# Optimization experiments

Measured on AMD Instinct MI355X. Metric: run time of the kernel, lower is better.

## Reference

```python
import jax, jax.numpy as jnp
import numpy as np

N_HEADS = 16

def setup_inputs() -> dict:
    key = jax.random.key(0)
    k1, k2, k3 = jax.random.split(key, 3)
    d = 1024
    x = jax.random.normal(k1, (2, 2048, d), dtype=jnp.float32)
    W_in = jax.random.normal(k2, (d, 3 * d), dtype=jnp.float32) * (d ** -0.5)
    W_out = jax.random.normal(k3, (d, d), dtype=jnp.float32) * (d ** -0.5)
    return {"x": x, "W_in": W_in, "W_out": W_out}

def reference(x, W_in, W_out):
    B, S, D = x.shape
    H = N_HEADS
    Dh = D // H
    qkv = x @ W_in                                  # [B,S,3D]
    q, k, v = jnp.split(qkv, 3, axis=-1)
    # [B,S,D] -> [B,H,S,Dh]
    q = q.reshape(B, S, H, Dh).transpose(0, 2, 1, 3)
    k = k.reshape(B, S, H, Dh).transpose(0, 2, 1, 3)
    v = v.reshape(B, S, H, Dh).transpose(0, 2, 1, 3)
    scores = jnp.einsum('bhqd,bhkd->bhqk', q, k)    # [B,H,S,S]
    causal = jnp.triu(jnp.ones((S, S), dtype=bool), k=1)
    scores = jnp.where(causal, -jnp.inf, scores)
    scores = scores / jnp.sqrt(jnp.asarray(Dh, scores.dtype))
    attn = jax.nn.softmax(scores, axis=-1)
    out = jnp.einsum('bhqk,bhkd->bhqd', attn, v)    # [B,H,S,Dh]
    out = out.transpose(0, 2, 1, 3).reshape(B, S, D)
    return out @ W_out
```

## Files before the change

### kernel.cpp

```cpp
#include <hip/hip_runtime.h>
#include <cstdint>
#include <cstddef>

typedef __bf16 bf16;
typedef bf16  bf16x4  __attribute__((ext_vector_type(4)));
typedef bf16  bf16x8  __attribute__((ext_vector_type(8)));
typedef float floatx4 __attribute__((ext_vector_type(4)));

#define BATCH 2
#define SEQ   2048
#define DIM   1024
#define NH    16
#define DH    64
#define D3    3072
#define MROWS 4096

__device__ __forceinline__ void gld16(void* lds, const void* gptr) {
  __builtin_amdgcn_global_load_lds(
      (const __attribute__((address_space(1))) unsigned int*)gptr,
      (__attribute__((address_space(3))) unsigned int*)lds, 16, 0, 0);
}

__global__ __launch_bounds__(256) void k_prep(const float4* __restrict__ x,
                                              bf16* __restrict__ xb,
                                              const float* __restrict__ Wi,
                                              bf16* __restrict__ wti,
                                              const float* __restrict__ Wo,
                                              bf16* __restrict__ wto) {
  __shared__ float tile[32][33];
  const int bid = blockIdx.x;
  if (bid < 4096) {
    int i = bid * 256 + threadIdx.x;
    float4 v = x[i];
    bf16x4 o;
    o.x = (bf16)v.x; o.y = (bf16)v.y; o.z = (bf16)v.z; o.w = (bf16)v.w;
    *(bf16x4*)(xb + (size_t)i * 4) = o;
    return;
  }
  const float* W; bf16* Wt; int N, id;
  if (bid < 7168) { W = Wi; Wt = wti; N = 3072; id = bid - 4096; }
  else            { W = Wo; Wt = wto; N = 1024; id = bid - 7168; }
  const int nb = N / 32;
  int n0 = (id % nb) * 32, k0 = (id / nb) * 32;
  int tx = threadIdx.x & 31, ty = threadIdx.x >> 5;
#pragma unroll
  for (int i = 0; i < 4; i++)
    tile[ty + i * 8][tx] = W[(size_t)(k0 + ty + i * 8) * N + n0 + tx];
  __syncthreads();
#pragma unroll
  for (int i = 0; i < 4; i++)
    Wt[(size_t)(n0 + ty + i * 8) * 1024 + k0 + tx] = (bf16)tile[tx][ty + i * 8];
}

__global__ __launch_bounds__(256, 2) void k_gemm1(const bf16* __restrict__ A,
                                                  const bf16* __restrict__ Bt,
                                                  bf16* __restrict__ qk,
                                                  bf16* __restrict__ vt) {
  constexpr int K = DIM;
  constexpr int nk = K / 64;
  __shared__ __align__(16) bf16 As[2][128 * 64];
  __shared__ __align__(16) bf16 Bs[2][192 * 64];

  const int t = threadIdx.x, l = t & 63, w = t >> 6;
  const int q = l >> 4, mm = l & 15;
  const int wm = w >> 1, wn = w & 1;

  const int xcd = blockIdx.x & 7, j = blockIdx.x >> 3;
  const int by = ((xcd >> 1) << 3) + (j >> 3);
  const int bx = ((xcd & 1) << 3) + (j & 7);
  const int m0 = by * 128, n0 = bx * 192;

  auto stA = [&](int T, int up) {
    const int bp = T & 1;
#pragma unroll
    for (int i = 0; i < 2; i++) {
      int c = t + i * 256;
      int rl = c >> 3, pos = c & 7;
      int row = ((rl >> 5) << 6) + (up << 5) + (rl & 31);
      int gs = pos ^ (row & 7);
      gld16((char*)(As[bp] + row * 64 + pos * 8),
            A + (size_t)(m0 + row) * K + T * 64 + gs * 8);
    }
  };
  auto stB = [&](int T, int up) {
    const int bp = T & 1;
#pragma unroll
    for (int i = 0; i < 3; i++) {
      int c = t + i * 256;
      int rl = c >> 3, pos = c & 7;
      int row = up * 96 + rl;
      int gs = pos ^ (row & 7);
      gld16((char*)(Bs[bp] + row * 64 + pos * 8),
            Bt + (size_t)(n0 + row) * K + T * 64 + gs * 8);
    }
  };

  floatx4 acc[4][6] = {};

  stA(0, 0); stB(0, 0); stA(0, 1); stB(0, 1);
  stA(1, 0); stB(1, 0);

  for (int T = 0; T < nk; T++) {
    const int bp = T & 1;
    if (T + 1 < nk)
      asm volatile("s_waitcnt vmcnt(5)\n\ts_barrier" ::: "memory");
    else
      asm volatile("s_waitcnt vmcnt(0)\n\ts_barrier" ::: "memory");

    const bf16* Ab = As[bp] + wm * 64 * 64;
    const bf16* Bb = Bs[bp] + wn * 96 * 64;
    bf16x8 a0[2][2], a1[2][2], b0[3][2], b1[3][2];

#pragma unroll
    for (int mt = 0; mt < 2; mt++)
#pragma unroll
      for (int kk = 0; kk < 2; kk++)
        a0[mt][kk] = *(const bf16x8*)(Ab + (size_t)(mt * 16 + mm) * 64 +
                                      ((kk * 4 + q) ^ (mm & 7)) * 8);
#pragma unroll
    for (int nt = 0; nt < 3; nt++)
#pragma unroll
      for (int kk = 0; kk < 2; kk++)
        b0[nt][kk] = *(const bf16x8*)(Bb + (size_t)(nt * 16 + mm) * 64 +
                                      ((kk * 4 + q) ^ (mm & 7)) * 8);
    if (T + 1 < nk) stA(T + 1, 1);
    asm volatile("s_barrier" ::: "memory");
    __builtin_amdgcn_s_setprio(1);
#pragma unroll
    for (int mt = 0; mt < 2; mt++)
#pragma unroll
      for (int nt = 0; nt < 3; nt++)
#pragma unroll
        for (int kk = 0; kk < 2; kk++)
          acc[mt][nt] = __builtin_amdgcn_mfma_f32_16x16x32_bf16(
              a0[mt][kk], b0[nt][kk], acc[mt][nt], 0, 0, 0);
    __builtin_amdgcn_s_setprio(0);
    asm volatile("s_barrier" ::: "memory");

#pragma unroll
    for (int nt = 0; nt < 3; nt++)
#pragma unroll
      for (int kk = 0; kk < 2; kk++)
        b1[nt][kk] = *(const bf16x8*)(Bb + (size_t)((3 + nt) * 16 + mm) * 64 +
                                      ((kk * 4 + q) ^ (mm & 7)) * 8);
    if (T + 1 < nk) stB(T + 1, 1);
    asm volatile("s_barrier" ::: "memory");
    __builtin_amdgcn_s_setprio(1);
#pragma unroll
    for (int mt = 0; mt < 2; mt++)
#pragma unroll
      for (int nt = 0; nt < 3; nt++)
#pragma unroll
        for (int kk = 0; kk < 2; kk++)
          acc[mt][3 + nt] = __builtin_amdgcn_mfma_f32_16x16x32_bf16(
              a0[mt][kk], b1[nt][kk], acc[mt][3 + nt], 0, 0, 0);
    __builtin_amdgcn_s_setprio(0);
    asm volatile("s_barrier" ::: "memory");

#pragma unroll
    for (int mt = 0; mt < 2; mt++)
#pragma unroll
      for (int kk = 0; kk < 2; kk++)
        a1[mt][kk] = *(const bf16x8*)(Ab + (size_t)(32 + mt * 16 + mm) * 64 +
                                      ((kk * 4 + q) ^ (mm & 7)) * 8);
    if (T + 2 < nk) stA(T + 2, 0);
    asm volatile("s_barrier" ::: "memory");
    __builtin_amdgcn_s_setprio(1);
#pragma unroll
    for (int mt = 0; mt < 2; mt++)
#pragma unroll
      for (int nt = 0; nt < 3; nt++)
#pragma unroll
        for (int kk = 0; kk < 2; kk++)
          acc[2 + mt][nt] = __builtin_amdgcn_mfma_f32_16x16x32_bf16(
              a1[mt][kk], b0[nt][kk], acc[2 + mt][nt], 0, 0, 0);
    __builtin_amdgcn_s_setprio(0);
    asm volatile("s_barrier" ::: "memory");

    if (T + 2 < nk) stB(T + 2, 0);
    asm volatile("s_barrier" ::: "memory");
    __builtin_amdgcn_s_setprio(1);
#pragma unroll
    for (int mt = 0; mt < 2; mt++)
#pragma unroll
      for (int nt = 0; nt < 3; nt++)
#pragma unroll
        for (int kk = 0; kk < 2; kk++)
          acc[2 + mt][3 + nt] = __builtin_amdgcn_mfma_f32_16x16x32_bf16(
              a1[mt][kk], b1[nt][kk], acc[2 + mt][3 + nt], 0, 0, 0);
    __builtin_amdgcn_s_setprio(0);
  }

#pragma unroll
  for (int mt = 0; mt < 4; mt++)
#pragma unroll
    for (int nt = 0; nt < 6; nt++) {
      int row = m0 + wm * 64 + mt * 16 + q * 4;
      int col = n0 + wn * 96 + nt * 16 + mm;
      if (col < 2048) {
#pragma unroll
        for (int r = 0; r < 4; r++)
          qk[(size_t)(row + r) * 2048 + col] = (bf16)acc[mt][nt][r];
      } else {
        int d = col - 2048;
        int hh = d >> 6, dh = d & 63;
#pragma unroll
        for (int r = 0; r < 4; r++) {
          int rr = row + r;
          int bb = rr >> 11, s = rr & 2047;
          vt[((size_t)(bb * 16 + hh) * 64 + dh) * SEQ + s] = (bf16)acc[mt][nt][r];
        }
      }
    }
}

__global__ __launch_bounds__(256, 2) void k_gemm2(const bf16* __restrict__ A,
                                                  const bf16* __restrict__ Bt,
                                                  float* __restrict__ C) {
  constexpr int K = DIM;
  constexpr int nk = K / 64;
  constexpr int N = DIM;
  __shared__ __align__(16) bf16 As[3][128 * 64];
  __shared__ __align__(16) bf16 Bs[3][64 * 64];

  const int t = threadIdx.x, l = t & 63, w = t >> 6;
  const int q = l >> 4, mm = l & 15;
  const int wm = w >> 1, wn = w & 1;

  const int xcd = blockIdx.x & 7, j = blockIdx.x >> 3;
  const int by = ((xcd >> 1) << 3) + (j >> 3);
  const int bx = ((xcd & 1) << 3) + (j & 7);
  const int m0 = by * 128, n0 = bx * 64;

  auto stA2 = [&](int T) {
    const int bp = T % 3;
#pragma unroll
    for (int i = 0; i < 4; i++) {
      int c = t + i * 256;
      int row = c >> 3, pos = c & 7;
      int gs = pos ^ (row & 7);
      gld16((char*)(As[bp] + row * 64 + pos * 8),
            A + (size_t)(m0 + row) * K + T * 64 + gs * 8);
    }
  };
  auto stB2 = [&](int T) {
    const int bp = T % 3;
#pragma unroll
    for (int i = 0; i < 2; i++) {
      int c = t + i * 256;
      int row = c >> 3, pos = c & 7;
      int gs = pos ^ (row & 7);
      gld16((char*)(Bs[bp] + row * 64 + pos * 8),
            Bt + (size_t)(n0 + row) * K + T * 64 + gs * 8);
    }
  };

  floatx4 acc[4][2] = {};

  stA2(0); stB2(0);
  stA2(1); stB2(1);

  for (int T = 0; T < nk; T++) {
    const int bp = T % 3;
    if (T + 1 < nk)
      asm volatile("s_waitcnt vmcnt(6)\n\ts_barrier" ::: "memory");
    else
      asm volatile("s_waitcnt vmcnt(0)\n\ts_barrier" ::: "memory");

    const bf16* Ab = As[bp] + wm * 64 * 64;
    const bf16* Bb = Bs[bp] + wn * 32 * 64;
    bf16x8 af[4][2], bf[2][2];

#pragma unroll
    for (int mt = 0; mt < 2; mt++)
#pragma unroll
      for (int kk = 0; kk < 2; kk++)
        af[mt][kk] = *(const bf16x8*)(Ab + (size_t)(mt * 16 + mm) * 64 +
                                      ((kk * 4 + q) ^ (mm & 7)) * 8);
#pragma unroll
    for (int nt = 0; nt < 2; nt++)
#pragma unroll
      for (int kk = 0; kk < 2; kk++)
        bf[nt][kk] = *(const bf16x8*)(Bb + (size_t)(nt * 16 + mm) * 64 +
                                      ((kk * 4 + q) ^ (mm & 7)) * 8);
    if (T + 2 < nk) stA2(T + 2);
    asm volatile("s_barrier" ::: "memory");
    __builtin_amdgcn_s_setprio(1);
#pragma unroll
    for (int mt = 0; mt < 2; mt++)
#pragma unroll
      for (int nt = 0; nt < 2; nt++)
#pragma unroll
        for (int kk = 0; kk < 2; kk++)
          acc[mt][nt] = __builtin_amdgcn_mfma_f32_16x16x32_bf16(
              af[mt][kk], bf[nt][kk], acc[mt][nt], 0, 0, 0);
    __builtin_amdgcn_s_setprio(0);
    asm volatile("s_barrier" ::: "memory");

#pragma unroll
    for (int mt = 0; mt < 2; mt++)
#pragma unroll
      for (int kk = 0; kk < 2; kk++)
        af[2 + mt][kk] = *(const bf16x8*)(Ab + (size_t)(32 + mt * 16 + mm) * 64 +
                                          ((kk * 4 + q) ^ (mm & 7)) * 8);
    if (T + 2 < nk) stB2(T + 2);
    asm volatile("s_barrier" ::: "memory");
    __builtin_amdgcn_s_setprio(1);
#pragma unroll
    for (int mt = 0; mt < 2; mt++)
#pragma unroll
      for (int nt = 0; nt < 2; nt++)
#pragma unroll
        for (int kk = 0; kk < 2; kk++)
          acc[2 + mt][nt] = __builtin_amdgcn_mfma_f32_16x16x32_bf16(
              af[2 + mt][kk], bf[nt][kk], acc[2 + mt][nt], 0, 0, 0);
    __builtin_amdgcn_s_setprio(0);
  }

#pragma unroll
  for (int mt = 0; mt < 4; mt++)
#pragma unroll
    for (int nt = 0; nt < 2; nt++) {
      int row = m0 + wm * 64 + mt * 16 + q * 4;
      int col = n0 + wn * 32 + nt * 16 + mm;
#pragma unroll
      for (int r = 0; r < 4; r++)
        C[(size_t)(row + r) * N + col] = acc[mt][nt][r];
    }
}

__global__ __launch_bounds__(256, 4) void k_attn(const bf16* __restrict__ qk,
                                                 const bf16* __restrict__ vt,
                                                 bf16* __restrict__ out) {
  const int bx = blockIdx.x;
  const int qt = 31 - (bx >> 5);
  const int bh = bx & 31;
  const int b = bh >> 4, h = bh & 15;
  const int t = threadIdx.x, l = t & 63, w = t >> 6;
  const int q4 = l >> 4, mm = l & 15;
  const int sw = (mm >> 1) & 3;

  __shared__ __align__(16) char lds[8192 + 16384 + 16384];
  bf16* Qs = (bf16*)lds;
  bf16* Ps = (bf16*)lds;
  bf16* Ks = (bf16*)(lds + 8192);
  bf16* Vs = (bf16*)(lds + 8192 + 16384);

  const size_t qkbase = (size_t)b * SEQ * 2048;
  const size_t vtbase = (size_t)bh * 64 * SEQ;

  auto stage = [&](int kt) {
    const int bp = kt & 1;
#pragma unroll
    for (int i = 0; i < 2; i++) {
      int row = t >> 2, pos = t & 3;
      int g = pos ^ ((row >> 1) & 3);
      gld16((char*)(Ks + bp * 4096) + ((size_t)t + i * 256) * 16,
            qk + qkbase + (size_t)(kt * 64 + row) * 2048 + 1024 + h * 64 + i * 32 + g * 8);
    }
#pragma unroll
    for (int i = 0; i < 2; i++) {
      int c = t + i * 256;
      int vr = c >> 3, vc = c & 7;
      int src = vc ^ (vr & 7);
      gld16((char*)(Vs + bp * 4096) + (size_t)c * 16,
            vt + vtbase + (size_t)vr * SEQ + kt * 64 + src * 8);
    }
  };

  {
    int row = t >> 2, col = (t & 3) * 8;
#pragma unroll
    for (int i = 0; i < 2; i++)
      gld16((char*)Qs + ((size_t)t + i * 256) * 16,
            qk + qkbase + (size_t)(qt * 64 + row) * 2048 + h * 64 + i * 32 + col);
  }
  stage(0);
  __syncthreads();
  bf16x8 qf[2];
#pragma unroll
  for (int ks = 0; ks < 2; ks++) {
    qf[ks] = *(const bf16x8*)(Qs + (size_t)(ks * 64 + w * 16 + mm) * 32 + q4 * 8);
#pragma unroll
    for (int j = 0; j < 8; j++)
      qf[ks][j] = (bf16)((float)qf[ks][j] * 0.18033688f);
  }
  __syncthreads();

  float l_i = 0.f;
  floatx4 oaccT[4] = {};
  const int qloc = w * 16 + mm;
  const float FM = 24.0f;

  bf16* Pw = Ps + (size_t)w * 640;

  for (int kt = 0; kt <= qt; kt++) {
    if (kt < qt) stage(kt + 1);
    const bf16* Kb = Ks + (kt & 1) * 4096;
    const bf16* Vb = Vs + (kt & 1) * 4096;

    floatx4 sacc[4] = {};
#pragma unroll
    for (int ks = 0; ks < 2; ks++)
#pragma unroll
      for (int ct = 0; ct < 4; ct++) {
        bf16x8 kf = *(const bf16x8*)(Kb + (size_t)(ks * 64 + ct * 16 + mm) * 32 + (q4 ^ sw) * 8);
        sacc[ct] = __builtin_amdgcn_mfma_f32_16x16x32_bf16(kf, qf[ks], sacc[ct], 0, 0, 0);
      }

    bf16x4 pk[4];
    float rsum = 0.f;
    if (kt == qt) {
#pragma unroll
      for (int ct = 0; ct < 4; ct++)
#pragma unroll
        for (int r = 0; r < 4; r++) {
          float e = (ct * 16 + q4 * 4 + r > qloc)
                        ? 0.f : __builtin_amdgcn_exp2f(sacc[ct][r] - FM);
          pk[ct][r] = (bf16)e;
          rsum += e;
        }
    } else {
#pragma unroll
      for (int ct = 0; ct < 4; ct++)
#pragma unroll
        for (int r = 0; r < 4; r++) {
          float e = __builtin_amdgcn_exp2f(sacc[ct][r] - FM);
          pk[ct][r] = (bf16)e;
          rsum += e;
        }
    }
    rsum += __shfl_xor(rsum, 16, 64);
    rsum += __shfl_xor(rsum, 32, 64);
    l_i += rsum;

#pragma unroll
    for (int ks = 0; ks < 2; ks++) {
      *(bf16x4*)(Pw + (size_t)mm * 40 + q4 * 4)      = pk[ks * 2 + 0];
      *(bf16x4*)(Pw + (size_t)mm * 40 + 16 + q4 * 4) = pk[ks * 2 + 1];
      bf16x8 pf = *(const bf16x8*)(Pw + (size_t)mm * 40 + q4 * 8);
#pragma unroll
      for (int nt = 0; nt < 4; nt++) {
        int chunk = (ks * 4 + q4) ^ (mm & 7);
        bf16x8 vf = *(const bf16x8*)(Vb + (size_t)(nt * 16 + mm) * 64 + chunk * 8);
        oaccT[nt] = __builtin_amdgcn_mfma_f32_16x16x32_bf16(vf, pf, oaccT[nt], 0, 0, 0);
      }
    }

    if (kt < qt) __syncthreads();
  }

  float inv = 1.0f / l_i;
  int qrow = qt * 64 + qloc;
  bf16* orow = out + ((size_t)b * SEQ + qrow) * DIM + h * 64;
#pragma unroll
  for (int nt = 0; nt < 4; nt++) {
    bf16x4 o4;
#pragma unroll
    for (int r = 0; r < 4; r++) o4[r] = (bf16)(oaccT[nt][r] * inv);
    *(bf16x4*)(orow + nt * 16 + q4 * 4) = o4;
  }
}

extern "C" void kernel_launch(void* const* d_in, const int* in_sizes, int n_in,
                              void* d_out, int out_size, void* d_ws, size_t ws_size,
                              hipStream_t stream) {
  const float* x     = (const float*)d_in[0];
  const float* W_in  = (const float*)d_in[1];
  const float* W_out = (const float*)d_in[2];
  float* out = (float*)d_out;

  char* ws = (char*)d_ws;
  bf16* xb   = (bf16*)(ws);
  bf16* wti  = (bf16*)(ws + 8388608);
  bf16* wto  = (bf16*)(ws + 14680064);
  bf16* qkb  = (bf16*)(ws + 16777216);
  bf16* vtb  = (bf16*)(ws + 33554432);
  bf16* attn = xb;

  k_prep<<<8192, 256, 0, stream>>>((const float4*)x, xb, W_in, wti, W_out, wto);
  k_gemm1<<<512, 256, 0, stream>>>(xb, wti, qkb, vtb);
  k_attn<<<1024, 256, 0, stream>>>(qkb, vtb, attn);
  k_gemm2<<<512, 256, 0, stream>>>(attn, wto, out);
}
```

Baseline: 156.6 us.

## Use 2 waves per attention block, each handling 32 query rows

The attention kernel now runs 128 threads (2 waves) per block instead of 4 waves, and each wave processes two 16-row query groups. Every K and V fragment read from shared memory is reused across both groups, halving LDS traffic per MFMA. The cost is more registers per wave, since accumulators and P tiles are doubled, plus fewer waves per block to hide latency, and each thread now issues twice as many global-to-LDS loads.

```diff
diff --git a/kernel.cpp b/kernel.cpp
--- a/kernel.cpp
+++ b/kernel.cpp
@@ -329,7 +329,7 @@
     }
 }
 
-__global__ __launch_bounds__(256, 4) void k_attn(const bf16* __restrict__ qk,
+__global__ __launch_bounds__(128, 2) void k_attn(const bf16* __restrict__ qk,
                                                  const bf16* __restrict__ vt,
                                                  bf16* __restrict__ out) {
   const int bx = blockIdx.x;
@@ -352,15 +352,16 @@
   auto stage = [&](int kt) {
     const int bp = kt & 1;
 #pragma unroll
-    for (int i = 0; i < 2; i++) {
-      int row = t >> 2, pos = t & 3;
+    for (int i = 0; i < 4; i++) {
+      int c = t + i * 128;
+      int ks = c >> 8, row = (c >> 2) & 63, pos = c & 3;
       int g = pos ^ ((row >> 1) & 3);
-      gld16((char*)(Ks + bp * 4096) + ((size_t)t + i * 256) * 16,
-            qk + qkbase + (size_t)(kt * 64 + row) * 2048 + 1024 + h * 64 + i * 32 + g * 8);
-    }
-#pragma unroll
-    for (int i = 0; i < 2; i++) {
-      int c = t + i * 256;
+      gld16((char*)(Ks + bp * 4096) + (size_t)c * 16,
+            qk + qkbase + (size_t)(kt * 64 + row) * 2048 + 1024 + h * 64 + ks * 32 + g * 8);
+    }
+#pragma unroll
+    for (int i = 0; i < 4; i++) {
+      int c = t + i * 128;
       int vr = c >> 3, vc = c & 7;
       int src = vc ^ (vr & 7);
       gld16((char*)(Vs + bp * 4096) + (size_t)c * 16,
@@ -369,96 +370,114 @@
   };
 
   {
-    int row = t >> 2, col = (t & 3) * 8;
-#pragma unroll
-    for (int i = 0; i < 2; i++)
-      gld16((char*)Qs + ((size_t)t + i * 256) * 16,
-            qk + qkbase + (size_t)(qt * 64 + row) * 2048 + h * 64 + i * 32 + col);
+#pragma unroll
+    for (int i = 0; i < 4; i++) {
+      int c = t + i * 128;
+      int ks = c >> 8, row = (c >> 2) & 63, pos = c & 3;
+      gld16((char*)Qs + (size_t)c * 16,
+            qk + qkbase + (size_t)(qt * 64 + row) * 2048 + h * 64 + ks * 32 + pos * 8);
+    }
   }
   stage(0);
   __syncthreads();
-  bf16x8 qf[2];
-#pragma unroll
-  for (int ks = 0; ks < 2; ks++) {
-    qf[ks] = *(const bf16x8*)(Qs + (size_t)(ks * 64 + w * 16 + mm) * 32 + q4 * 8);
-#pragma unroll
-    for (int j = 0; j < 8; j++)
-      qf[ks][j] = (bf16)((float)qf[ks][j] * 0.18033688f);
-  }
+  bf16x8 qf[2][2];
+#pragma unroll
+  for (int g = 0; g < 2; g++)
+#pragma unroll
+    for (int ks = 0; ks < 2; ks++) {
+      qf[g][ks] = *(const bf16x8*)(Qs + (size_t)(ks * 64 + w * 32 + g * 16 + mm) * 32 + q4 * 8);
+#pragma unroll
+      for (int j = 0; j < 8; j++)
+        qf[g][ks][j] = (bf16)((float)qf[g][ks][j] * 0.18033688f);
+    }
   __syncthreads();
 
-  float l_i = 0.f;
-  floatx4 oaccT[4] = {};
-  const int qloc = w * 16 + mm;
+  float l_i[2] = {0.f, 0.f};
+  floatx4 oaccT[2][4] = {};
   const float FM = 24.0f;
 
-  bf16* Pw = Ps + (size_t)w * 640;
+  bf16* Pw0 = Ps + (size_t)(w * 2 + 0) * 640;
+  bf16* Pw1 = Ps + (size_t)(w * 2 + 1) * 640;
 
   for (int kt = 0; kt <= qt; kt++) {
     if (kt < qt) stage(kt + 1);
     const bf16* Kb = Ks + (kt & 1) * 4096;
     const bf16* Vb = Vs + (kt & 1) * 4096;
 
-    floatx4 sacc[4] = {};
+    floatx4 sacc[2][4] = {};
 #pragma unroll
     for (int ks = 0; ks < 2; ks++)
 #pragma unroll
       for (int ct = 0; ct < 4; ct++) {
         bf16x8 kf = *(const bf16x8*)(Kb + (size_t)(ks * 64 + ct * 16 + mm) * 32 + (q4 ^ sw) * 8);
-        sacc[ct] = __builtin_amdgcn_mfma_f32_16x16x32_bf16(kf, qf[ks], sacc[ct], 0, 0, 0);
+        sacc[0][ct] = __builtin_amdgcn_mfma_f32_16x16x32_bf16(kf, qf[0][ks], sacc[0][ct], 0, 0, 0);
+        sacc[1][ct] = __builtin_amdgcn_mfma_f32_16x16x32_bf16(kf, qf[1][ks], sacc[1][ct], 0, 0, 0);
       }
 
-    bf16x4 pk[4];
-    float rsum = 0.f;
+    bf16x4 pk[2][4];
+    float rs0 = 0.f, rs1 = 0.f;
     if (kt == qt) {
+      const int ql0 = w * 32 + mm, ql1 = w * 32 + 16 + mm;
 #pragma unroll
       for (int ct = 0; ct < 4; ct++)
 #pragma unroll
         for (int r = 0; r < 4; r++) {
-          float e = (ct * 16 + q4 * 4 + r > qloc)
-                        ? 0.f : __builtin_amdgcn_exp2f(sacc[ct][r] - FM);
-          pk[ct][r] = (bf16)e;
-          rsum += e;
+          int kv = ct * 16 + q4 * 4 + r;
+          float e0 = (kv > ql0) ? 0.f : __builtin_amdgcn_exp2f(sacc[0][ct][r] - FM);
+          float e1 = (kv > ql1) ? 0.f : __builtin_amdgcn_exp2f(sacc[1][ct][r] - FM);
+          pk[0][ct][r] = (bf16)e0; rs0 += e0;
+          pk[1][ct][r] = (bf16)e1; rs1 += e1;
         }
     } else {
 #pragma unroll
       for (int ct = 0; ct < 4; ct++)
 #pragma unroll
         for (int r = 0; r < 4; r++) {
-          float e = __builtin_amdgcn_exp2f(sacc[ct][r] - FM);
-          pk[ct][r] = (bf16)e;
-          rsum += e;
+          float e0 = __builtin_amdgcn_exp2f(sacc[0][ct][r] - FM);
+          float e1 = __builtin_amdgcn_exp2f(sacc[1][ct][r] - FM);
+          pk[0][ct][r] = (bf16)e0; rs0 += e0;
+          pk[1][ct][r] = (bf16)e1; rs1 += e1;
         }
     }
-    rsum += __shfl_xor(rsum, 16, 64);
-    rsum += __shfl_xor(rsum, 32, 64);
-    l_i += rsum;
+    rs0 += __shfl_xor(rs0, 16, 64);
+    rs0 += __shfl_xor(rs0, 32, 64);
+    rs1 += __shfl_xor(rs1, 16, 64);
+    rs1 += __shfl_xor(rs1, 32, 64);
+    l_i[0] += rs0;
+    l_i[1] += rs1;
 
 #pragma unroll
     for (int ks = 0; ks < 2; ks++) {
-      *(bf16x4*)(Pw + (size_t)mm * 40 + q4 * 4)      = pk[ks * 2 + 0];
-      *(bf16x4*)(Pw + (size_t)mm * 40 + 16 + q4 * 4) = pk[ks * 2 + 1];
-      bf16x8 pf = *(const bf16x8*)(Pw + (size_t)mm * 40 + q4 * 8);
+      *(bf16x4*)(Pw0 + (size_t)mm * 40 + q4 * 4)      = pk[0][ks * 2 + 0];
+      *(bf16x4*)(Pw0 + (size_t)mm * 40 + 16 + q4 * 4) = pk[0][ks * 2 + 1];
+      *(bf16x4*)(Pw1 + (size_t)mm * 40 + q4 * 4)      = pk[1][ks * 2 + 0];
+      *(bf16x4*)(Pw1 + (size_t)mm * 40 + 16 + q4 * 4) = pk[1][ks * 2 + 1];
+      bf16x8 pf0 = *(const bf16x8*)(Pw0 + (size_t)mm * 40 + q4 * 8);
+      bf16x8 pf1 = *(const bf16x8*)(Pw1 + (size_t)mm * 40 + q4 * 8);
 #pragma unroll
       for (int nt = 0; nt < 4; nt++) {
         int chunk = (ks * 4 + q4) ^ (mm & 7);
         bf16x8 vf = *(const bf16x8*)(Vb + (size_t)(nt * 16 + mm) * 64 + chunk * 8);
-        oaccT[nt] = __builtin_amdgcn_mfma_f32_16x16x32_bf16(vf, pf, oaccT[nt], 0, 0, 0);
+        oaccT[0][nt] = __builtin_amdgcn_mfma_f32_16x16x32_bf16(vf, pf0, oaccT[0][nt], 0, 0, 0);
+        oaccT[1][nt] = __builtin_amdgcn_mfma_f32_16x16x32_bf16(vf, pf1, oaccT[1][nt], 0, 0, 0);
       }
     }
 
     if (kt < qt) __syncthreads();
   }
 
-  float inv = 1.0f / l_i;
-  int qrow = qt * 64 + qloc;
-  bf16* orow = out + ((size_t)b * SEQ + qrow) * DIM + h * 64;
-#pragma unroll
-  for (int nt = 0; nt < 4; nt++) {
-    bf16x4 o4;
-#pragma unroll
-    for (int r = 0; r < 4; r++) o4[r] = (bf16)(oaccT[nt][r] * inv);
-    *(bf16x4*)(orow + nt * 16 + q4 * 4) = o4;
+#pragma unroll
+  for (int g = 0; g < 2; g++) {
+    float inv = 1.0f / l_i[g];
+    int qrow = qt * 64 + w * 32 + g * 16 + mm;
+    bf16* orow = out + ((size_t)b * SEQ + qrow) * DIM + h * 64;
+#pragma unroll
+    for (int nt = 0; nt < 4; nt++) {
+      bf16x4 o4;
+#pragma unroll
+      for (int r = 0; r < 4; r++) o4[r] = (bf16)(oaccT[g][nt][r] * inv);
+      *(bf16x4*)(orow + nt * 16 + q4 * 4) = o4;
+    }
   }
 }
 
@@ -480,6 +499,6 @@
 
   k_prep<<<8192, 256, 0, stream>>>((const float4*)x, xb, W_in, wti, W_out, wto);
   k_gemm1<<<512, 256, 0, stream>>>(xb, wti, qkb, vtb);
-  k_attn<<<1024, 256, 0, stream>>>(qkb, vtb, attn);
+  k_attn<<<1024, 128, 0, stream>>>(qkb, vtb, attn);
   k_gemm2<<<512, 256, 0, stream>>>(attn, wto, out);
 }
```

Measured after the change: 160.7 us. 2.6% more time.
